# Optimization experiments

Hardware: AMD Instinct MI355X
Metric: run time of the kernel (lower is better)

The kernel has to match this reference:

```python
import jax, jax.numpy as jnp
import numpy as np

D_MODEL = 256
NUM_TYPES = 7
B, N = 2, 512


def setup_inputs() -> dict:
    key = jax.random.key(0)
    k1, k2, k3 = jax.random.split(key, 3)
    lane_features = jax.random.normal(k1, (B, N, D_MODEL), dtype=jnp.float32)
    # nn.Linear(2D, D): weight [D, 2D], bias [D]; stored transposed for x @ W
    s1 = 1.0 / np.sqrt(2 * D_MODEL)
    W1 = jax.random.uniform(k2, (2 * D_MODEL, D_MODEL), minval=-s1, maxval=s1, dtype=jnp.float32)
    b1 = jnp.zeros((D_MODEL,), dtype=jnp.float32)
    s2 = 1.0 / np.sqrt(D_MODEL)
    W2 = jax.random.uniform(k3, (D_MODEL, NUM_TYPES), minval=-s2, maxval=s2, dtype=jnp.float32)
    b2 = jnp.zeros((NUM_TYPES,), dtype=jnp.float32)
    return {"lane_features": lane_features, "W1": W1, "b1": b1, "W2": W2, "b2": b2}


def reference(lane_features, W1, b1, W2, b2):
    # cat([lane_i, lane_j]) @ W1 == lane_i @ W1[:D] + lane_j @ W1[D:]
    D = lane_features.shape[-1]
    W1a, W1b = W1[:D], W1[D:]
    hi = lane_features @ W1a            # [B, N, D]
    hj = lane_features @ W1b            # [B, N, D]
    h = hi[:, :, None, :] + hj[:, None, :, :] + b1  # [B, N, N, D]
    h = jax.nn.relu(h)                  # dropout is identity at inference
    logits = h @ W2 + b2                # [B, N, N, NUM_TYPES]
    return logits
```

## Files before the change

kernel.cpp:

```cpp
#include <hip/hip_runtime.h>

#define D_MODEL   256
#define NUM_TYPES 7
#define BATCH     2
#define NLANES    512
#define LSTR      264

typedef _Float16  f16x8   __attribute__((ext_vector_type(8)));
typedef float     floatx4 __attribute__((ext_vector_type(4)));


__global__ __launch_bounds__(256) void k1_mfma(
    const float* __restrict__ x, const float* __restrict__ W1,
    const float* __restrict__ b1, const float* __restrict__ W2,
    _Float16* __restrict__ Hi16, _Float16* __restrict__ Hj16,
    _Float16* __restrict__ w2f)
{
    __shared__ __align__(16) _Float16 xs[64][LSTR];

    const int tid  = threadIdx.x, lane = tid & 63, w = tid >> 6;
    const int nt   = blockIdx.x;
    const int half = nt >> 4;
    const int nc   = (nt & 15) * 16;
    const int r0   = blockIdx.y * 64;
    const int jr   = lane & 15, g = lane >> 4, ks = g * 8;

    {
        const float4* xsrc = (const float4*)(x + (size_t)r0 * D_MODEL);
        #pragma unroll
        for (int q = 0; q < 8; ++q) {
            const int gg = q * 512 + tid * 2;
            const int r  = gg >> 6;
            const int c4 = gg & 63;
            const float4 v0 = xsrc[gg];
            const float4 v1 = xsrc[gg + 1];
            f16x8 o;
            o[0] = (_Float16)v0.x; o[1] = (_Float16)v0.y;
            o[2] = (_Float16)v0.z; o[3] = (_Float16)v0.w;
            o[4] = (_Float16)v1.x; o[5] = (_Float16)v1.y;
            o[6] = (_Float16)v1.z; o[7] = (_Float16)v1.w;
            *(f16x8*)&xs[r][c4 * 4] = o;
        }
    }

    f16x8 w1f[8];
    {
        const float* wb = W1 + (size_t)(half * D_MODEL + ks) * D_MODEL + nc + jr;
        #pragma unroll
        for (int kc = 0; kc < 8; ++kc)
            #pragma unroll
            for (int e = 0; e < 8; ++e)
                w1f[kc][e] = (_Float16)wb[(size_t)(kc * 32 + e) * D_MODEL];
    }

    __syncthreads();

    floatx4 acc = {0.f, 0.f, 0.f, 0.f};
    #pragma unroll
    for (int kc = 0; kc < 8; ++kc) {
        const f16x8 a = *(const f16x8*)&xs[w * 16 + jr][kc * 32 + ks];
        acc = __builtin_amdgcn_mfma_f32_16x16x32_f16(a, w1f[kc], acc, 0, 0, 0);
    }

    _Float16* Hb = half ? Hj16 : Hi16;
    const float bias = half ? 0.f : b1[nc + jr];
    const int m0 = r0 + w * 16;
    #pragma unroll
    for (int r = 0; r < 4; ++r)
        Hb[(size_t)(m0 + g * 4 + r) * D_MODEL + nc + jr] = (_Float16)(acc[r] + bias);

    if (nt == 0 && blockIdx.y == 0) {
        #pragma unroll
        for (int s0 = 0; s0 < 2; ++s0) {
            const int s   = tid + s0 * 256;
            const int l2  = s & 63, kc2 = s >> 6;
            const int t2  = l2 & 15, ks2 = (l2 >> 4) * 8;
            f16x8 frag;
            #pragma unroll
            for (int e = 0; e < 8; ++e) {
                const int k = kc2 * 32 + ks2 + e;
                frag[e] = (t2 < NUM_TYPES)
                    ? (_Float16)W2[(size_t)k * NUM_TYPES + t2] : (_Float16)0.f;
            }
            *(f16x8*)(w2f + (size_t)s * 8) = frag;
        }
    }
}

__global__ __launch_bounds__(256, 3) void k2_pair(
    const _Float16* __restrict__ Hi16, const _Float16* __restrict__ Hj16,
    const _Float16* __restrict__ w2f, const float* __restrict__ b2,
    float* __restrict__ out)
{
    __shared__ _Float16 hs[48][LSTR];

    const int tid  = threadIdx.x;
    const int lane = tid & 63, w = tid >> 6;
    const int b    = blockIdx.z;
    const int j0   = blockIdx.x * 32;
    const int i0   = blockIdx.y * 16;
    const int jr   = lane & 15, g = lane >> 4, ks = g * 8;

    #pragma unroll
    for (int q = 0; q < 2; ++q) {
        const int gg = tid + q * 256;
        const int r  = gg >> 5;
        const int c  = (gg & 31) * 8;
        *(f16x8*)&hs[r][c] = *(const f16x8*)(
            Hi16 + (size_t)(b * NLANES + i0 + r) * D_MODEL + c);
    }
    #pragma unroll
    for (int q = 0; q < 4; ++q) {
        const int gg = tid + q * 256;
        const int r  = gg >> 5;
        const int c  = (gg & 31) * 8;
        *(f16x8*)&hs[16 + r][c] = *(const f16x8*)(
            Hj16 + (size_t)(b * NLANES + j0 + r) * D_MODEL + c);
    }

    const int tb = g * 4;
    float bias2[4];
    #pragma unroll
    for (int r = 0; r < 4; ++r)
        bias2[r] = (tb + r < NUM_TYPES) ? b2[tb + r] : 0.f;

    __syncthreads();

    const int ig = w;
    const f16x8* w2fp = (const f16x8*)w2f + lane;

    floatx4 acc[4][2];
    #pragma unroll
    for (int u = 0; u < 4; ++u)
        #pragma unroll
        for (int jg = 0; jg < 2; ++jg)
            acc[u][jg] = (floatx4){0.f, 0.f, 0.f, 0.f};

    #pragma unroll
    for (int kch = 0; kch < 2; ++kch) {
        const int kb = kch * 128;

        f16x8 w2h[4];
        #pragma unroll
        for (int kc = 0; kc < 4; ++kc)
            w2h[kc] = w2fp[(kch * 4 + kc) * 64];

        f16x8 hj[2][4];
        #pragma unroll
        for (int jg = 0; jg < 2; ++jg)
            #pragma unroll
            for (int kc = 0; kc < 4; ++kc)
                hj[jg][kc] = *(const f16x8*)&hs[16 + jg * 16 + jr][kb + kc * 32 + ks];

        f16x8 hi[4][4];
        #pragma unroll
        for (int u = 0; u < 4; ++u)
            #pragma unroll
            for (int kc = 0; kc < 4; ++kc)
                hi[u][kc] = *(const f16x8*)&hs[ig * 4 + u][kb + kc * 32 + ks];

        #pragma unroll
        for (int u = 0; u < 4; ++u)
            #pragma unroll
            for (int kc = 0; kc < 4; ++kc) {
                const f16x8 z = {};
                f16x8 s0 = __builtin_elementwise_max(hi[u][kc] + hj[0][kc], z);
                acc[u][0] = __builtin_amdgcn_mfma_f32_16x16x32_f16(
                    w2h[kc], s0, acc[u][0], 0, 0, 0);
                f16x8 s1 = __builtin_elementwise_max(hi[u][kc] + hj[1][kc], z);
                acc[u][1] = __builtin_amdgcn_mfma_f32_16x16x32_f16(
                    w2h[kc], s1, acc[u][1], 0, 0, 0);
            }
    }

    if (lane < 32) {
        #pragma unroll
        for (int u = 0; u < 4; ++u) {
            const int i = i0 + ig * 4 + u;
            #pragma unroll
            for (int jg = 0; jg < 2; ++jg) {
                const floatx4 a = acc[u][jg];
                const int j = j0 + jg * 16 + jr;
                float* op = out + ((size_t)(b * NLANES + i) * NLANES + j) * NUM_TYPES + tb;
                if (tb == 0) {
                    float v4[4] = { a[0] + bias2[0], a[1] + bias2[1],
                                    a[2] + bias2[2], a[3] + bias2[3] };
                    __builtin_memcpy(op, v4, 16);
                } else {
                    float v2[2] = { a[0] + bias2[0], a[1] + bias2[1] };
                    __builtin_memcpy(op, v2, 8);
                    op[2] = a[2] + bias2[2];
                }
            }
        }
    }
}

extern "C" void kernel_launch(void* const* d_in, const int* in_sizes, int n_in,
                              void* d_out, int out_size, void* d_ws, size_t ws_size,
                              hipStream_t stream) {
    const float* x  = (const float*)d_in[0];
    const float* W1 = (const float*)d_in[1];
    const float* b1 = (const float*)d_in[2];
    const float* W2 = (const float*)d_in[3];
    const float* b2 = (const float*)d_in[4];
    float* out = (float*)d_out;

    char* ws = (char*)d_ws;
    _Float16* Hi16 = (_Float16*)ws;
    _Float16* Hj16 = (_Float16*)(ws + 512u * 1024u);
    _Float16* w2f  = (_Float16*)(ws + 1024u * 1024u);

    k1_mfma<<<dim3(32, 16), 256, 0, stream>>>(x, W1, b1, W2, Hi16, Hj16, w2f);
    k2_pair<<<dim3(NLANES / 32, NLANES / 16, BATCH), 256, 0, stream>>>(
        Hi16, Hj16, w2f, b2, out);
}
```

Before: 20.01 us.

## Process two j-tiles per block with register prefetch of next Hj tile

Each k2 block now handles 64 j columns in two 32-wide passes, reusing the staged Hi tile. The second Hj tile is prefetched into registers during the first pass and written to shared memory between passes. This halves the grid size and the block-startup and Hi reload costs, and the launch bound rises to 4 blocks per CU. The risks are higher register pressure from the prefetch and less parallelism from the smaller grid (512 blocks).

```diff
diff --git a/kernel.cpp b/kernel.cpp
--- a/kernel.cpp
+++ b/kernel.cpp
@@ -87,7 +87,7 @@
     }
 }
 
-__global__ __launch_bounds__(256, 3) void k2_pair(
+__global__ __launch_bounds__(256, 4) void k2_pair(
     const _Float16* __restrict__ Hi16, const _Float16* __restrict__ Hj16,
     const _Float16* __restrict__ w2f, const float* __restrict__ b2,
     float* __restrict__ out)
@@ -97,25 +97,24 @@
     const int tid  = threadIdx.x;
     const int lane = tid & 63, w = tid >> 6;
     const int b    = blockIdx.z;
-    const int j0   = blockIdx.x * 32;
+    const int jc   = blockIdx.x;
     const int i0   = blockIdx.y * 16;
     const int jr   = lane & 15, g = lane >> 4, ks = g * 8;
 
+    const int sr = tid >> 5;
+    const int sc = (tid & 31) * 8;
+
     #pragma unroll
     for (int q = 0; q < 2; ++q) {
-        const int gg = tid + q * 256;
-        const int r  = gg >> 5;
-        const int c  = (gg & 31) * 8;
-        *(f16x8*)&hs[r][c] = *(const f16x8*)(
-            Hi16 + (size_t)(b * NLANES + i0 + r) * D_MODEL + c);
+        const int r = sr + q * 8;
+        *(f16x8*)&hs[r][sc] = *(const f16x8*)(
+            Hi16 + (size_t)(b * NLANES + i0 + r) * D_MODEL + sc);
     }
     #pragma unroll
     for (int q = 0; q < 4; ++q) {
-        const int gg = tid + q * 256;
-        const int r  = gg >> 5;
-        const int c  = (gg & 31) * 8;
-        *(f16x8*)&hs[16 + r][c] = *(const f16x8*)(
-            Hj16 + (size_t)(b * NLANES + j0 + r) * D_MODEL + c);
+        const int r = sr + q * 8;
+        *(f16x8*)&hs[16 + r][sc] = *(const f16x8*)(
+            Hj16 + (size_t)(b * NLANES + jc * 64 + r) * D_MODEL + sc);
     }
 
     const int tb = g * 4;
@@ -126,72 +125,93 @@
 
     __syncthreads();
 
+    f16x8 pj[4];
+    #pragma unroll
+    for (int q = 0; q < 4; ++q) {
+        const int r = sr + q * 8;
+        pj[q] = *(const f16x8*)(
+            Hj16 + (size_t)(b * NLANES + jc * 64 + 32 + r) * D_MODEL + sc);
+    }
+
     const int ig = w;
     const f16x8* w2fp = (const f16x8*)w2f + lane;
 
-    floatx4 acc[4][2];
-    #pragma unroll
-    for (int u = 0; u < 4; ++u)
-        #pragma unroll
-        for (int jg = 0; jg < 2; ++jg)
-            acc[u][jg] = (floatx4){0.f, 0.f, 0.f, 0.f};
-
-    #pragma unroll
-    for (int kch = 0; kch < 2; ++kch) {
-        const int kb = kch * 128;
-
-        f16x8 w2h[4];
-        #pragma unroll
-        for (int kc = 0; kc < 4; ++kc)
-            w2h[kc] = w2fp[(kch * 4 + kc) * 64];
-
-        f16x8 hj[2][4];
-        #pragma unroll
-        for (int jg = 0; jg < 2; ++jg)
+    #pragma unroll 1
+    for (int tt = 0; tt < 2; ++tt) {
+        const int j0 = jc * 64 + tt * 32;
+
+        floatx4 acc[4][2];
+        #pragma unroll
+        for (int u = 0; u < 4; ++u)
+            #pragma unroll
+            for (int jg = 0; jg < 2; ++jg)
+                acc[u][jg] = (floatx4){0.f, 0.f, 0.f, 0.f};
+
+        #pragma unroll
+        for (int kch = 0; kch < 2; ++kch) {
+            const int kb = kch * 128;
+
+            f16x8 w2h[4];
             #pragma unroll
             for (int kc = 0; kc < 4; ++kc)
-                hj[jg][kc] = *(const f16x8*)&hs[16 + jg * 16 + jr][kb + kc * 32 + ks];
-
-        f16x8 hi[4][4];
-        #pragma unroll
-        for (int u = 0; u < 4; ++u)
-            #pragma unroll
-            for (int kc = 0; kc < 4; ++kc)
-                hi[u][kc] = *(const f16x8*)&hs[ig * 4 + u][kb + kc * 32 + ks];
-
-        #pragma unroll
-        for (int u = 0; u < 4; ++u)
-            #pragma unroll
-            for (int kc = 0; kc < 4; ++kc) {
-                const f16x8 z = {};
-                f16x8 s0 = __builtin_elementwise_max(hi[u][kc] + hj[0][kc], z);
-                acc[u][0] = __builtin_amdgcn_mfma_f32_16x16x32_f16(
-                    w2h[kc], s0, acc[u][0], 0, 0, 0);
-                f16x8 s1 = __builtin_elementwise_max(hi[u][kc] + hj[1][kc], z);
-                acc[u][1] = __builtin_amdgcn_mfma_f32_16x16x32_f16(
-                    w2h[kc], s1, acc[u][1], 0, 0, 0);
-            }
-    }
-
-    if (lane < 32) {
-        #pragma unroll
-        for (int u = 0; u < 4; ++u) {
-            const int i = i0 + ig * 4 + u;
-            #pragma unroll
-            for (int jg = 0; jg < 2; ++jg) {
-                const floatx4 a = acc[u][jg];
-                const int j = j0 + jg * 16 + jr;
-                float* op = out + ((size_t)(b * NLANES + i) * NLANES + j) * NUM_TYPES + tb;
-                if (tb == 0) {
-                    float v4[4] = { a[0] + bias2[0], a[1] + bias2[1],
-                                    a[2] + bias2[2], a[3] + bias2[3] };
-                    __builtin_memcpy(op, v4, 16);
-                } else {
-                    float v2[2] = { a[0] + bias2[0], a[1] + bias2[1] };
-                    __builtin_memcpy(op, v2, 8);
-                    op[2] = a[2] + bias2[2];
+                w2h[kc] = w2fp[(kch * 4 + kc) * 64];
+
+            f16x8 hj[2][4];
+            #pragma unroll
+            for (int jg = 0; jg < 2; ++jg)
+                #pragma unroll
+                for (int kc = 0; kc < 4; ++kc)
+                    hj[jg][kc] = *(const f16x8*)&hs[16 + jg * 16 + jr][kb + kc * 32 + ks];
+
+            f16x8 hi[4][4];
+            #pragma unroll
+            for (int u = 0; u < 4; ++u)
+                #pragma unroll
+                for (int kc = 0; kc < 4; ++kc)
+                    hi[u][kc] = *(const f16x8*)&hs[ig * 4 + u][kb + kc * 32 + ks];
+
+            #pragma unroll
+            for (int u = 0; u < 4; ++u)
+                #pragma unroll
+                for (int kc = 0; kc < 4; ++kc) {
+                    const f16x8 z = {};
+                    f16x8 s0 = __builtin_elementwise_max(hi[u][kc] + hj[0][kc], z);
+                    acc[u][0] = __builtin_amdgcn_mfma_f32_16x16x32_f16(
+                        w2h[kc], s0, acc[u][0], 0, 0, 0);
+                    f16x8 s1 = __builtin_elementwise_max(hi[u][kc] + hj[1][kc], z);
+                    acc[u][1] = __builtin_amdgcn_mfma_f32_16x16x32_f16(
+                        w2h[kc], s1, acc[u][1], 0, 0, 0);
+                }
+        }
+
+        if (lane < 32) {
+            #pragma unroll
+            for (int u = 0; u < 4; ++u) {
+                const int i = i0 + ig * 4 + u;
+                #pragma unroll
+                for (int jg = 0; jg < 2; ++jg) {
+                    const floatx4 a = acc[u][jg];
+                    const int j = j0 + jg * 16 + jr;
+                    float* op = out + ((size_t)(b * NLANES + i) * NLANES + j) * NUM_TYPES + tb;
+                    if (tb == 0) {
+                        float v4[4] = { a[0] + bias2[0], a[1] + bias2[1],
+                                        a[2] + bias2[2], a[3] + bias2[3] };
+                        __builtin_memcpy(op, v4, 16);
+                    } else {
+                        float v2[2] = { a[0] + bias2[0], a[1] + bias2[1] };
+                        __builtin_memcpy(op, v2, 8);
+                        op[2] = a[2] + bias2[2];
+                    }
                 }
             }
+        }
+
+        if (tt == 0) {
+            __syncthreads();
+            #pragma unroll
+            for (int q = 0; q < 4; ++q)
+                *(f16x8*)&hs[16 + sr + q * 8][sc] = pj[q];
+            __syncthreads();
         }
     }
 }
@@ -212,6 +232,5 @@
     _Float16* w2f  = (_Float16*)(ws + 1024u * 1024u);
 
     k1_mfma<<<dim3(32, 16), 256, 0, stream>>>(x, W1, b1, W2, Hi16, Hj16, w2f);
-    k2_pair<<<dim3(NLANES / 32, NLANES / 16, BATCH), 256, 0, stream>>>(
-        Hi16, Hj16, w2f, b2, out);
+    k2_pair<<<dim3(8, 32, BATCH), 256, 0, stream>>>(Hi16, Hj16, w2f, b2, out);
 }
```

After: 24.88 us. 1.24x slower.
